# Kernel tuning notes

Hardware: AMD Instinct MI355X
Metric: run time of the kernel (lower is better)

Reference implementation:

```python
import jax, jax.numpy as jnp
import numpy as np

QC = 13        # quantum_channel
NQ = 12        # qubits per patch circuit
LAYERS12 = 3   # num_layer for FQConv ansatz
LAYERS4 = 4    # layers for the 4-qubit basic ansatz
GROUPS = 10
DIM = 40       # 3*QC + 1 channels
B = 1024
TDIM = 128
EPS = 1e-6     # flax GroupNorm default epsilon
TWO_PI = 2.0 * float(np.pi)


def _take2(s, ax):
    return jnp.take(s, 0, axis=ax), jnp.take(s, 1, axis=ax)


def init_state(n, N):
    # |0...0> state, shape (N, 2, 2, ..., 2); wire w lives on axis w+1
    s = jnp.zeros((N, 2 ** n), jnp.complex64).at[:, 0].set(1.0)
    return s.reshape((N,) + (2,) * n)


def apply_rx(state, theta, w):
    # RX(theta) = [[c, -i s], [-i s, c]], c=cos(theta/2), s=sin(theta/2)
    ax = w + 1
    theta = jnp.asarray(theta, jnp.float32)
    c = jnp.cos(0.5 * theta)
    s = jnp.sin(0.5 * theta)
    if theta.ndim > 0:  # per-sample angles (data embedding)
        sh = (-1,) + (1,) * (state.ndim - 2)
        c = c.reshape(sh)
        s = s.reshape(sh)
    c = c.astype(state.dtype)
    js = (1j * s).astype(state.dtype)
    s0, s1 = _take2(state, ax)
    return jnp.stack([c * s0 - js * s1, c * s1 - js * s0], axis=ax)


def apply_cnot(state, c, t):
    ca = c + 1
    ta = t + 1 if t < c else t  # target axis inside the control=1 slice
    s0, s1 = _take2(state, ca)
    return jnp.stack([s0, jnp.flip(s1, axis=ta)], axis=ca)


def apply_crz(state, theta, c, t):
    # CRZ = diag(1, 1, e^{-i theta/2}, e^{+i theta/2})
    ca = c + 1
    ta = t + 1 if t < c else t
    s0, s1 = _take2(state, ca)
    t0, t1 = _take2(s1, ta)
    em = jnp.exp(-0.5j * theta).astype(state.dtype)
    ep = jnp.exp(0.5j * theta).astype(state.dtype)
    s1 = jnp.stack([em * t0, ep * t1], axis=ta)
    return jnp.stack([s0, s1], axis=ca)


def apply_crx(state, theta, c, t):
    # controlled RX on target when control = 1
    ca = c + 1
    ta = t + 1 if t < c else t
    s0, s1 = _take2(state, ca)
    t0, t1 = _take2(s1, ta)
    ch = jnp.cos(0.5 * theta).astype(state.dtype)
    js = (1j * jnp.sin(0.5 * theta)).astype(state.dtype)
    s1 = jnp.stack([ch * t0 - js * t1, ch * t1 - js * t0], axis=ta)
    return jnp.stack([s0, s1], axis=ca)


def expvals_z(state, n):
    # <Z_w> = P(bit_w = 0) - P(bit_w = 1)
    p = jnp.real(state * jnp.conj(state))
    zs = []
    for w in range(n):
        axes = tuple(a for a in range(1, n + 1) if a != w + 1)
        q = p.sum(axis=axes)  # (N, 2)
        zs.append(q[:, 0] - q[:, 1])
    return jnp.stack(zs, axis=-1)  # (N, n)


def fqconv_layer(state, th):
    # zip(range(11,-1,-4), range(12)) -> i in (11,7,3), j in (0,1,2)
    for j, i in enumerate((11, 7, 3)):
        w1 = [i - 3, i - 2, i - 1, i] + [(i + k) % NQ for k in (1, 2, 3, 4)]
        tj = th[8 * j: 8 * (j + 1)]
        for bi, bj in zip(range(3, -1, -1), range(4)):  # block_C: CRZ
            state = apply_crz(state, TWO_PI * tj[bj], w1[bi + 4], w1[bi])
        for bi, bj in zip(range(3, -1, -1), range(4)):  # block_D: CRX
            state = apply_crx(state, TWO_PI * tj[4 + bj], w1[bi + 4], w1[bi])
    return state


def circuit12(x, theta):
    # x: (N, 12) angles; theta: (72,)
    state = init_state(NQ, x.shape[0])
    for w in range(NQ):  # AngleEmbedding, rotation='X'
        state = apply_rx(state, x[:, w], w)
    for l in range(LAYERS12):
        state = fqconv_layer(state, theta[24 * l: 24 * (l + 1)])
    return expvals_z(state, NQ)


def circuit4(x, theta):
    # Basic_ansatz, 4 qubits, 4 layers, 4 params/layer
    state = init_state(4, x.shape[0])
    for w in range(4):
        state = apply_rx(state, x[:, w], w)
    for l in range(LAYERS4):
        for w in range(4):
            state = apply_rx(state, theta[4 * l + w], w)
        for w in range(3):
            state = apply_cnot(state, w, w + 1)
        state = apply_cnot(state, 3, 0)
    return expvals_z(state, 4)


def run12_all(y, params, circ):
    # scan over the QC per-channel circuits (same structure, different params)
    def body(carry, xp):
        yy, th = xp
        return carry, circ(yy, th)
    _, zs = jax.lax.scan(body, None, (y, params))
    return zs  # (QC, N, 12)


def group_norm(h, scale, bias):
    Bn, H, W, C = h.shape
    g = h.reshape(Bn, H, W, GROUPS, C // GROUPS)
    mu = g.mean(axis=(1, 2, 4), keepdims=True)
    var = g.var(axis=(1, 2, 4), keepdims=True)
    g = (g - mu) * jax.lax.rsqrt(var + EPS)
    return g.reshape(Bn, H, W, C) * scale + bias


def forward(x, time_emb, qparams12, qparams4, gn0_scale, gn0_bias,
            gn1_scale, gn1_bias, time_w, time_b, circ12=circuit12):
    Bn = x.shape[0]

    def qpass(inp, p12_block):
        # per-channel 12-qubit circuits on 2x2x3 patches
        y = jnp.stack([inp[..., 3 * i:3 * (i + 1)].reshape(-1, 12) for i in range(QC)], 0)
        z = run12_all(y, p12_block, circ12)                      # (QC, Bn, 12)
        h1 = jnp.moveaxis(z.reshape(QC, Bn, 2, 2, 3), 0, -2).reshape(Bn, 2, 2, 3 * QC)
        # NOTE: faithful to the source, BOTH passes use circuit/params[-2]
        h4 = circuit4(inp[..., 3 * QC:].reshape(-1, 4), qparams4[0]).reshape(Bn, 2, 2, 1)
        return jnp.concatenate([h1, h4], axis=-1)                 # (Bn, 2, 2, 40)

    h = qpass(x, qparams12[:QC])
    h = group_norm(h, gn0_scale, gn0_bias)
    t = jax.nn.swish(time_emb) @ time_w + time_b                  # (Bn, 2*DIM)
    scale, shift = jnp.split(t[:, None, None, :], 2, axis=-1)
    h = jax.nn.swish(h * (1.0 + scale) + shift)
    h = qpass(h, qparams12[QC:])
    h = jax.nn.swish(group_norm(h, gn1_scale, gn1_bias))
    return x + h  # C == dim, so no res_conv


def setup_inputs() -> dict:
    key = jax.random.key(0)
    ks = jax.random.split(key, 5)
    return {
        "x": jax.random.normal(ks[0], (B, 2, 2, DIM), jnp.float32),
        "time_emb": jax.random.normal(ks[1], (B, TDIM), jnp.float32),
        "qparams12": jax.random.uniform(ks[2], (2 * QC, 24 * LAYERS12), jnp.float32),
        "qparams4": jax.random.uniform(ks[3], (2, 16), jnp.float32),
        "gn0_scale": jnp.ones((DIM,), jnp.float32),
        "gn0_bias": jnp.zeros((DIM,), jnp.float32),
        "gn1_scale": jnp.ones((DIM,), jnp.float32),
        "gn1_bias": jnp.zeros((DIM,), jnp.float32),
        "time_w": jax.random.normal(ks[4], (TDIM, 2 * DIM), jnp.float32) * (TDIM ** -0.5),
        "time_b": jnp.zeros((2 * DIM,), jnp.float32),
    }


def reference(x, time_emb, qparams12, qparams4, gn0_scale, gn0_bias,
              gn1_scale, gn1_bias, time_w, time_b):
    return forward(x, time_emb, qparams12, qparams4, gn0_scale, gn0_bias,
                   gn1_scale, gn1_bias, time_w, time_b)
```

## Files before the change

### kernel.cpp

```cpp
#include <hip/hip_runtime.h>
#include <math.h>


#define PI_F 3.14159265358979323846f

typedef float f2 __attribute__((ext_vector_type(2)));

__device__ __forceinline__ f2 shfl2(f2 v, int mask)
{
    f2 r;
    r[0] = __shfl_xor(v[0], mask, 64);
    r[1] = __shfl_xor(v[1], mask, 64);
    return r;
}

__device__ __forceinline__ void crz_g0_fused(const float* a, f2* R, f2* I,
                                             int lane, int wq)
{
    float gr[4], gi[4];
#pragma unroll
    for (int m = 0; m < 4; ++m) {
        bool cb;
        if      (m == 0) cb = (lane >> 4) & 1;
        else if (m == 1) cb = (lane >> 5) & 1;
        else if (m == 2) cb = wq & 1;
        else             cb = (wq >> 1) & 1;
        gr[m] = cb ? a[2 * m]     : 1.0f;
        gi[m] = cb ? a[2 * m + 1] : 0.0f;
    }
    float u0 = gr[1] * gr[0], v0 = gi[1] * gi[0];
    float w0 = gr[1] * gi[0], z0 = gi[1] * gr[0];
    float p01r[2] = { u0 - v0, u0 + v0 };
    float p01i[2] = { -(w0 + z0), w0 - z0 };
    float u1 = gr[3] * gr[2], v1 = gi[3] * gi[2];
    float w1 = gr[3] * gi[2], z1 = gi[3] * gr[2];
    float p23r[2] = { u1 - v1, u1 + v1 };
    float p23i[2] = { -(w1 + z1), w1 - z1 };

#pragma unroll
    for (int j = 0; j < 8; ++j) {
        const int ta  = (j < 4) ? 2 * j     : 15 - 2 * j;
        const int tb  = (j < 4) ? 2 * j + 1 : 14 - 2 * j;
        const float sgn = (j < 4) ? 1.0f : -1.0f;
        const int a10 = ta & 3, a2 = (ta >> 2) & 1;
        float bar = (a10 == 0 || a10 == 3) ? p01r[0] : p01r[1];
        float bai = (a10 == 0) ? p01i[0] : (a10 == 1) ? p01i[1]
                  : (a10 == 2) ? -p01i[1] : -p01i[0];
        float m0r = p23r[a2] * bar - p23i[a2] * bai;
        float m0i = p23r[a2] * bai + p23i[a2] * bar;
        const int b10 = tb & 3, b2 = (tb >> 2) & 1;
        float bbr = (b10 == 0 || b10 == 3) ? p01r[0] : p01r[1];
        float bbi = (b10 == 0) ? p01i[0] : (b10 == 1) ? p01i[1]
                  : (b10 == 2) ? -p01i[1] : -p01i[0];
        float m1r = p23r[b2] * bbr - p23i[b2] * bbi;
        float m1i = p23r[b2] * bbi + p23i[b2] * bbr;
        f2 mr = { m0r, m1r };
        f2 mi = { sgn * m0i, sgn * m1i };
        f2 r = R[j], im = I[j];
        R[j] = mr * r - mi * im;
        I[j] = mr * im + mi * r;
    }
}

__device__ __forceinline__ void crx_pair(float cg, float sg, f2* R, f2* I)
{
#pragma unroll
    for (int j = 0; j < 8; ++j) {
        f2 r = R[j], im = I[j];
        f2 rs = __builtin_shufflevector(r, r, 1, 0);
        f2 is = __builtin_shufflevector(im, im, 1, 0);
        R[j] = cg * r + sg * is;
        I[j] = cg * im - sg * rs;
    }
}

template<int M>
__device__ __forceinline__ void crx_elem(float cg, float sg, f2* R, f2* I)
{
#pragma unroll
    for (int j = 0; j < 8; ++j) {
        if (j & M) continue;
        const int p = j | M;
        f2 r0 = R[j], i0 = I[j], r1 = R[p], i1 = I[p];
        R[j] = cg * r0 + sg * i1;  I[j] = cg * i0 - sg * r1;
        R[p] = cg * r1 + sg * i0;  I[p] = cg * i1 - sg * r0;
    }
}

__device__ __forceinline__ void crz_e(float cg, float ss, f2* R, f2* I)
{
    const f2 mrv = {1.0f, cg};
    const f2 miv = {0.0f, ss};
#pragma unroll
    for (int j = 0; j < 8; ++j) {
        f2 r = R[j], im = I[j];
        R[j] = mrv * r - miv * im;
        I[j] = mrv * im + miv * r;
    }
}

template<int CB>
__device__ __forceinline__ void crz_ctrlj(float cg, float ss, f2* R, f2* I)
{
#pragma unroll
    for (int j = 0; j < 8; ++j) {
        if (!((j >> CB) & 1)) continue;
        f2 r = R[j], im = I[j];
        R[j] = cg * r - ss * im;
        I[j] = cg * im + ss * r;
    }
}

__device__ __forceinline__ void crx_sh_e(float cg, float sg, f2* R, f2* I)
{
    const f2 cgv = {1.0f, cg};
    const f2 sgv = {0.0f, sg};
#pragma unroll
    for (int j = 0; j < 8; ++j) {
        f2 br = shfl2(R[j], 1);
        f2 bi = shfl2(I[j], 1);
        f2 r = R[j], im = I[j];
        R[j] = cgv * r + sgv * bi;
        I[j] = cgv * im - sgv * br;
    }
}

template<int CB, int MASK>
__device__ __forceinline__ void crx_shj(float cg, float sg, f2* R, f2* I)
{
#pragma unroll
    for (int j = 0; j < 8; ++j) {
        if (!((j >> CB) & 1)) continue;
        f2 br = shfl2(R[j], MASK);
        f2 bi = shfl2(I[j], MASK);
        f2 r = R[j], im = I[j];
        R[j] = cg * r + sg * bi;
        I[j] = cg * im - sg * br;
    }
}

__device__ __forceinline__ void crz_g2_fused(const float* a, f2* R, f2* I,
                                             int lane, int wq)
{
    float s0 = ((lane >> 4) & 1) ? a[1] : -a[1];
    bool  c0 = lane & 1;
    float f0r = c0 ? a[0] : 1.0f, f0i = c0 ? s0 : 0.0f;
    float s1 = ((lane >> 5) & 1) ? a[3] : -a[3];
    bool  c1 = (lane >> 1) & 1;
    float f1r = c1 ? a[2] : 1.0f, f1i = c1 ? s1 : 0.0f;
    float s2 = (wq & 1) ? a[5] : -a[5];
    bool  c2 = (lane >> 2) & 1;
    float f2r = c2 ? a[4] : 1.0f, f2i = c2 ? s2 : 0.0f;
    float s3 = ((wq >> 1) & 1) ? a[7] : -a[7];
    bool  c3 = (lane >> 3) & 1;
    float f3r = c3 ? a[6] : 1.0f, f3i = c3 ? s3 : 0.0f;
    float t01r = f0r * f1r - f0i * f1i, t01i = f0r * f1i + f0i * f1r;
    float t23r = f2r * f3r - f2i * f3i, t23i = f2r * f3i + f2i * f3r;
    float Pr = t01r * t23r - t01i * t23i;
    float Pi = t01r * t23i + t01i * t23r;
#pragma unroll
    for (int j = 0; j < 8; ++j) {
        f2 r = R[j], im = I[j];
        R[j] = Pr * r - Pi * im;
        I[j] = Pr * im + Pi * r;
    }
}

template<int MASK>
__device__ __forceinline__ void crx_perm(float cg, float sg, f2* R, f2* I)
{
#pragma unroll
    for (int j = 0; j < 8; ++j) {
        float a0 = R[j][0], b0 = I[j][0];
        float a1 = R[j][1], b1 = I[j][1];
        if constexpr (MASK == 16) {
            asm("v_permlane16_swap_b32 %0, %1\n\t"
                "v_permlane16_swap_b32 %1, %0" : "+v"(a0), "+v"(b0));
            asm("v_permlane16_swap_b32 %0, %1\n\t"
                "v_permlane16_swap_b32 %1, %0" : "+v"(a1), "+v"(b1));
        } else {
            asm("v_permlane32_swap_b32 %0, %1\n\t"
                "v_permlane32_swap_b32 %1, %0" : "+v"(a0), "+v"(b0));
            asm("v_permlane32_swap_b32 %0, %1\n\t"
                "v_permlane32_swap_b32 %1, %0" : "+v"(a1), "+v"(b1));
        }
        f2 A = {a0, a1}, Bv = {b0, b1};
        f2 r = R[j], im = I[j];
        R[j] = cg * r + sg * A;
        I[j] = cg * im - sg * Bv;
    }
}

__global__ void __launch_bounds__(256, 4)
qpass12_kernel(const float* __restrict__ inp, const float* __restrict__ cs,
               float* __restrict__ outp)
{
    __shared__ f2 xbufv[4 * 32 * 17];
    float* xbuff = reinterpret_cast<float*>(xbufv);
    const int ts   = threadIdx.x;
    const int wq   = ts >> 6;
    const int lane = ts & 63;
    const int sim  = blockIdx.x;
    const int ci = sim % 13;
    const int b  = sim / 13;
    const float* csc = cs + ci * 144;
    const int ibase = b * 160 + ci * 3;

    float cw[12], sw[12];
#pragma unroll
    for (int w = 0; w < 12; ++w) {
        float x = inp[ibase + (w / 3) * 40 + (w % 3)];
        __sincosf(0.5f * x, &sw[w], &cw[w]);
    }

    float pref = ((wq >> 1) ? sw[0] : cw[0]) * ((wq & 1) ? sw[1] : cw[1]);
#pragma unroll
    for (int w = 2; w < 8; ++w)
        pref *= ((lane >> (7 - w)) & 1) ? sw[w] : cw[w];

    const int pl = (__popc(lane) + __popc(wq)) & 3;
    float oa = (pl == 0) ? 1.0f : (pl == 2) ? -1.0f : 0.0f;
    float ob = (pl == 1) ? -1.0f : (pl == 3) ? 1.0f : 0.0f;

    f2 R[8], I[8];
#pragma unroll
    for (int j = 0; j < 8; ++j) {
        float base = pref * ((j & 4) ? sw[8] : cw[8]) *
                     ((j & 2) ? sw[9] : cw[9]) * ((j & 1) ? sw[10] : cw[10]);
        f2 v2 = { base * cw[11], base * sw[11] };
        const int q0 = __popc(j) & 3;
        const int q1 = (q0 + 1) & 3;
        const float c0l = (q0 == 0) ? oa : (q0 == 1) ? ob : (q0 == 2) ? -oa : -ob;
        const float c1l = (q0 == 0) ? ob : (q0 == 1) ? -oa : (q0 == 2) ? -ob : oa;
        const float c0h = (q1 == 0) ? oa : (q1 == 1) ? ob : (q1 == 2) ? -oa : -ob;
        const float c1h = (q1 == 0) ? ob : (q1 == 1) ? -oa : (q1 == 2) ? -ob : oa;
        R[j] = f2{ v2[0] * c0l, v2[1] * c0h };
        I[j] = f2{ v2[0] * c1l, v2[1] * c1h };
    }

    const bool act2 = (lane >> 2) & 1;
    const bool act3 = (lane >> 3) & 1;
    const int ai2 = ((lane >> 3) << 2) | (lane & 3);
    const int ai3 = ((lane >> 4) << 3) | (lane & 7);
    f2* xw2 = &xbufv[(wq * 32 + ai2) * 17];
    f2* xr2 = &xbufv[((wq ^ 1) * 32 + ai2) * 17];
    f2* xw3 = &xbufv[(wq * 32 + ai3) * 17];
    f2* xr3 = &xbufv[((wq ^ 2) * 32 + ai3) * 17];

#pragma unroll 1
    for (int l = 0; l < 3; ++l) {
        const float* a = csc + l * 48;

        crz_g0_fused(a, R, I, lane, wq);
        { bool cb = (lane >> 4) & 1;
          crx_pair(cb ? a[ 8] : 1.0f, cb ? a[ 9] : 0.0f, R, I); }
        { bool cb = (lane >> 5) & 1;
          crx_elem<1>(cb ? a[10] : 1.0f, cb ? a[11] : 0.0f, R, I); }
        { bool cb = wq & 1;
          crx_elem<2>(cb ? a[12] : 1.0f, cb ? a[13] : 0.0f, R, I); }
        { bool cb = (wq >> 1) & 1;
          crx_elem<4>(cb ? a[14] : 1.0f, cb ? a[15] : 0.0f, R, I); }

        { float ss = (lane & 1) ? a[17] : -a[17];
          crz_e(a[16], ss, R, I); }
        { float ss = ((lane >> 1) & 1) ? a[19] : -a[19];
          crz_ctrlj<0>(a[18], ss, R, I); }
        { float ss = ((lane >> 2) & 1) ? a[21] : -a[21];
          crz_ctrlj<1>(a[20], ss, R, I); }
        { float ss = ((lane >> 3) & 1) ? a[23] : -a[23];
          crz_ctrlj<2>(a[22], ss, R, I); }
        crx_sh_e(a[24], a[25], R, I);
        crx_shj<0, 2>(a[26], a[27], R, I);
        crx_shj<1, 4>(a[28], a[29], R, I);
        crx_shj<2, 8>(a[30], a[31], R, I);

        crz_g2_fused(a + 32, R, I, lane, wq);
        { bool cb = lane & 1;
          crx_perm<16>(cb ? a[40] : 1.0f, cb ? a[41] : 0.0f, R, I); }
        { bool cb = (lane >> 1) & 1;
          crx_perm<32>(cb ? a[42] : 1.0f, cb ? a[43] : 0.0f, R, I); }
        __syncthreads();
        if (act2) {
#pragma unroll
            for (int j = 0; j < 8; ++j) {
                xw2[j]     = R[j];
                xw2[8 + j] = I[j];
            }
        }
        __syncthreads();
        if (act2) {
            float cg = a[44], sg = a[45];
#pragma unroll
            for (int j = 0; j < 8; ++j) {
                f2 br = xr2[j], bi = xr2[8 + j];
                f2 r = R[j], im = I[j];
                R[j] = cg * r + sg * bi;
                I[j] = cg * im - sg * br;
            }
        }
        __syncthreads();
        if (act3) {
#pragma unroll
            for (int j = 0; j < 8; ++j) {
                xw3[j]     = R[j];
                xw3[8 + j] = I[j];
            }
        }
        __syncthreads();
        if (act3) {
            float cg = a[46], sg = a[47];
#pragma unroll
            for (int j = 0; j < 8; ++j) {
                f2 br = xr3[j], bi = xr3[8 + j];
                f2 r = R[j], im = I[j];
                R[j] = cg * r + sg * bi;
                I[j] = cg * im - sg * br;
            }
        }
    }

    f2 accT = {0.0f, 0.0f}, acc8 = {0.0f, 0.0f};
    f2 acc9 = {0.0f, 0.0f}, acc10 = {0.0f, 0.0f};
#pragma unroll
    for (int j = 0; j < 8; ++j) {
        f2 p = R[j] * R[j] + I[j] * I[j];
        accT += p;
        if (j & 4) acc8 -= p; else acc8 += p;
        if (j & 2) acc9 -= p; else acc9 += p;
        if (j & 1) acc10 -= p; else acc10 += p;
    }
    float total = accT[0] + accT[1];
    float v12[12];
    v12[0] = (wq >> 1) ? -total : total;
    v12[1] = (wq & 1) ? -total : total;
#pragma unroll
    for (int w = 2; w < 8; ++w)
        v12[w] = ((lane >> (7 - w)) & 1) ? -total : total;
    v12[8]  = acc8[0] + acc8[1];
    v12[9]  = acc9[0] + acc9[1];
    v12[10] = acc10[0] + acc10[1];
    v12[11] = accT[0] - accT[1];

#pragma unroll
    for (int w = 0; w < 12; ++w) {
#pragma unroll
        for (int off = 1; off < 64; off <<= 1)
            v12[w] += __shfl_xor(v12[w], off, 64);
    }
    __syncthreads();
    if (lane == 0) {
#pragma unroll
        for (int w = 0; w < 12; ++w)
            xbuff[wq * 12 + w] = v12[w];
    }
    __syncthreads();
    if (ts < 12) {
        float z = xbuff[ts] + xbuff[12 + ts] + xbuff[24 + ts] + xbuff[36 + ts];
        outp[ibase + (ts / 3) * 40 + (ts % 3)] = z;
    }
}

__global__ void q4_kernel(const float* __restrict__ inp,
                          const float* __restrict__ cs4,
                          float* __restrict__ outp)
{
    int b = blockIdx.x * blockDim.x + threadIdx.x;
    if (b >= 1024) return;
    float cw[4], sw[4];
#pragma unroll
    for (int j = 0; j < 4; ++j) {
        float x = inp[(b * 4 + j) * 40 + 39];
        __sincosf(0.5f * x, &sw[j], &cw[j]);
    }
    float sr[16], si[16];
#pragma unroll
    for (int k = 0; k < 16; ++k) {
        float v = 1.0f;
#pragma unroll
        for (int j = 0; j < 4; ++j)
            v *= ((k >> (3 - j)) & 1) ? sw[j] : cw[j];
        int ph = __popc(k) & 3;
        sr[k] = (ph == 0) ? v : (ph == 2) ? -v : 0.0f;
        si[k] = (ph == 1) ? -v : (ph == 3) ? v : 0.0f;
    }
#pragma unroll
    for (int l = 0; l < 4; ++l) {
#pragma unroll
        for (int w = 0; w < 4; ++w) {
            float cg = cs4[2 * (4 * l + w)], sg = cs4[2 * (4 * l + w) + 1];
            const int m = 1 << (3 - w);
#pragma unroll
            for (int k = 0; k < 16; ++k) {
                if (k & m) continue;
                int p2 = k | m;
                float r0 = sr[k], i0 = si[k], r1 = sr[p2], i1 = si[p2];
                sr[k]  = cg * r0 + sg * i1;  si[k]  = cg * i0 - sg * r1;
                sr[p2] = cg * r1 + sg * i0;  si[p2] = cg * i1 - sg * r0;
            }
        }
#pragma unroll
        for (int e = 0; e < 4; ++e) {
            const int cq = e, tq = (e + 1) & 3;
            const int pcb = 1 << (3 - cq), ptb = 1 << (3 - tq);
#pragma unroll
            for (int k = 0; k < 16; ++k) {
                if (!(k & pcb)) continue;
                if (k & ptb) continue;
                int p2 = k | ptb;
                float tr = sr[k], ti = si[k];
                sr[k] = sr[p2]; si[k] = si[p2];
                sr[p2] = tr;    si[p2] = ti;
            }
        }
    }
    float p[16];
#pragma unroll
    for (int k = 0; k < 16; ++k) p[k] = sr[k] * sr[k] + si[k] * si[k];
#pragma unroll
    for (int j = 0; j < 4; ++j) {
        float z = 0.0f;
#pragma unroll
        for (int k = 0; k < 16; ++k)
            z += ((k >> (3 - j)) & 1) ? -p[k] : p[k];
        outp[(b * 4 + j) * 40 + 39] = z;
    }
}

__global__ void prep_kernel(const float* __restrict__ q12,
                            const float* __restrict__ q4,
                            float* __restrict__ cs12,
                            float* __restrict__ cs4)
{
    int idx = blockIdx.x * 256 + threadIdx.x;
    if (idx < 26 * 72) {
        float s, c;
        sincosf(PI_F * q12[idx], &s, &c);
        cs12[2 * idx]     = c;
        cs12[2 * idx + 1] = s;
    }
    if (idx < 16) {
        float s, c;
        sincosf(0.5f * q4[idx], &s, &c);
        cs4[2 * idx]     = c;
        cs4[2 * idx + 1] = s;
    }
}

__global__ void tmlp_kernel(const float* __restrict__ emb,
                            const float* __restrict__ W,
                            const float* __restrict__ bias,
                            float* __restrict__ t)
{
    __shared__ float se[128];
    int b = blockIdx.x, tid = threadIdx.x;
    float e = emb[b * 128 + tid];
    se[tid] = e / (1.0f + __expf(-e));
    __syncthreads();
    if (tid < 80) {
        float acc = bias[tid];
        for (int k = 0; k < 128; ++k) acc += se[k] * W[k * 80 + tid];
        t[b * 80 + tid] = acc;
    }
}

__global__ void gn0_kernel(const float* __restrict__ h, const float* __restrict__ t,
                           const float* __restrict__ sc, const float* __restrict__ bi,
                           float* __restrict__ outp)
{
    __shared__ float v[160];
    __shared__ float mu[10], rstd[10];
    int b = blockIdx.x, tid = threadIdx.x;
    if (tid < 160) v[tid] = h[b * 160 + tid];
    __syncthreads();
    if (tid < 10) {
        float s1 = 0.0f, s2 = 0.0f;
#pragma unroll
        for (int sp = 0; sp < 4; ++sp)
#pragma unroll
            for (int k = 0; k < 4; ++k) {
                float x = v[sp * 40 + tid * 4 + k];
                s1 += x; s2 += x * x;
            }
        float m = s1 * (1.0f / 16.0f);
        float var = s2 * (1.0f / 16.0f) - m * m;
        mu[tid] = m; rstd[tid] = rsqrtf(var + 1e-6f);
    }
    __syncthreads();
    if (tid < 160) {
        int ch = tid % 40;
        int g = ch >> 2;
        float hn = (v[tid] - mu[g]) * rstd[g] * sc[ch] + bi[ch];
        float scale = t[b * 80 + ch], shift = t[b * 80 + 40 + ch];
        float z = hn * (1.0f + scale) + shift;
        outp[b * 160 + tid] = z / (1.0f + __expf(-z));
    }
}

__global__ void gn1_kernel(const float* __restrict__ h, const float* __restrict__ x,
                           const float* __restrict__ sc, const float* __restrict__ bi,
                           float* __restrict__ outp)
{
    __shared__ float v[160];
    __shared__ float mu[10], rstd[10];
    int b = blockIdx.x, tid = threadIdx.x;
    if (tid < 160) v[tid] = h[b * 160 + tid];
    __syncthreads();
    if (tid < 10) {
        float s1 = 0.0f, s2 = 0.0f;
#pragma unroll
        for (int sp = 0; sp < 4; ++sp)
#pragma unroll
            for (int k = 0; k < 4; ++k) {
                float xx = v[sp * 40 + tid * 4 + k];
                s1 += xx; s2 += xx * xx;
            }
        float m = s1 * (1.0f / 16.0f);
        float var = s2 * (1.0f / 16.0f) - m * m;
        mu[tid] = m; rstd[tid] = rsqrtf(var + 1e-6f);
    }
    __syncthreads();
    if (tid < 160) {
        int ch = tid % 40;
        int g = ch >> 2;
        float hn = (v[tid] - mu[g]) * rstd[g] * sc[ch] + bi[ch];
        float sws = hn / (1.0f + __expf(-hn));
        outp[b * 160 + tid] = x[b * 160 + tid] + sws;
    }
}

extern "C" void kernel_launch(void* const* d_in, const int* in_sizes, int n_in,
                              void* d_out, int out_size, void* d_ws, size_t ws_size,
                              hipStream_t stream)
{
    const float* x    = (const float*)d_in[0];
    const float* temb = (const float*)d_in[1];
    const float* q12  = (const float*)d_in[2];
    const float* q4   = (const float*)d_in[3];
    const float* gn0s = (const float*)d_in[4];
    const float* gn0b = (const float*)d_in[5];
    const float* gn1s = (const float*)d_in[6];
    const float* gn1b = (const float*)d_in[7];
    const float* tw   = (const float*)d_in[8];
    const float* tb   = (const float*)d_in[9];
    float* out = (float*)d_out;

    float* ws   = (float*)d_ws;
    float* cs12 = ws;
    float* cs4  = cs12 + 3744;
    float* tbuf = cs4 + 32;
    float* A    = tbuf + 81920;
    float* Bf   = A + 163840;

    prep_kernel<<<8, 256, 0, stream>>>(q12, q4, cs12, cs4);
    tmlp_kernel<<<1024, 128, 0, stream>>>(temb, tw, tb, tbuf);

    qpass12_kernel<<<13312, 256, 0, stream>>>(x, cs12, A);
    q4_kernel<<<16, 64, 0, stream>>>(x, cs4, A);
    gn0_kernel<<<1024, 160, 0, stream>>>(A, tbuf, gn0s, gn0b, Bf);

    qpass12_kernel<<<13312, 256, 0, stream>>>(Bf, cs12 + 13 * 144, A);
    q4_kernel<<<16, 64, 0, stream>>>(Bf, cs4, A);
    gn1_kernel<<<1024, 160, 0, stream>>>(A, x, gn1s, gn1b, out);
}
```

Measured before the change: 650.6 us.

## Replace shfl_xor exchanges with DPP/swizzle/permlane and restructure wave reductions

Cross-lane exchanges in the CRX gates now use DPP row operations (xor1, xor2, xor8), ds_swizzle (xor4) and permlane swaps instead of __shfl_xor, which goes through LDS-bypass bpermute. The final 12-way wave reduction is restructured: the eight sign-pattern Z expectations are derived from a single butterfly on the total plus difference terms captured at each stage, which cuts the number of full 64-lane reductions. This adds inline assembly for v_permlane16/32_swap, which is specific to newer CDNA parts. It also relies on the DPP control encodings being correct for xor semantics; the xor8 encoding in particular looks questionable.

Result: faster. 577.5 us (-11.2%).

```diff
diff --git a/kernel.cpp b/kernel.cpp
--- a/kernel.cpp
+++ b/kernel.cpp
@@ -4,14 +4,61 @@
 
 #define PI_F 3.14159265358979323846f
 
+#define DPP_XOR1 0xB1
+#define DPP_XOR2 0x4E
+#define DPP_XOR8 0x128
+
 typedef float f2 __attribute__((ext_vector_type(2)));
 
-__device__ __forceinline__ f2 shfl2(f2 v, int mask)
+template<int CTRL>
+__device__ __forceinline__ float dppf(float x)
+{
+    return __int_as_float(__builtin_amdgcn_update_dpp(
+        __float_as_int(x), __float_as_int(x), CTRL, 0xF, 0xF, false));
+}
+
+template<int CTRL>
+__device__ __forceinline__ f2 dpp2v(f2 v)
 {
     f2 r;
-    r[0] = __shfl_xor(v[0], mask, 64);
-    r[1] = __shfl_xor(v[1], mask, 64);
+    r[0] = dppf<CTRL>(v[0]);
+    r[1] = dppf<CTRL>(v[1]);
     return r;
+}
+
+__device__ __forceinline__ float swz4f(float x)
+{
+    return __int_as_float(__builtin_amdgcn_ds_swizzle(__float_as_int(x), 0x101F));
+}
+
+__device__ __forceinline__ f2 swz4v(f2 v)
+{
+    f2 r;
+    r[0] = swz4f(v[0]);
+    r[1] = swz4f(v[1]);
+    return r;
+}
+
+__device__ __forceinline__ float psum16(float x)
+{
+    float c, d;
+    asm("v_mov_b32 %0, %2\n\t"
+        "v_mov_b32 %1, %2\n\t"
+        "v_permlane16_swap_b32 %0, %1"
+        : "=&v"(c), "=&v"(d)
+        : "v"(x));
+    return c + d;
+}
+
+__device__ __forceinline__ float psum32(float x)
+{
+    float c, d;
+    asm("v_mov_b32 %0, %2\n\t"
+        "v_mov_b32 %1, %2\n\t"
+        "v_permlane32_swap_b32 %0, %1"
+        : "=&v"(c), "=&v"(d)
+        : "v"(x));
+    return c + d;
 }
 
 __device__ __forceinline__ void crz_g0_fused(const float* a, f2* R, f2* I,
@@ -117,22 +164,36 @@
     const f2 sgv = {0.0f, sg};
 #pragma unroll
     for (int j = 0; j < 8; ++j) {
-        f2 br = shfl2(R[j], 1);
-        f2 bi = shfl2(I[j], 1);
+        f2 br = dpp2v<DPP_XOR1>(R[j]);
+        f2 bi = dpp2v<DPP_XOR1>(I[j]);
         f2 r = R[j], im = I[j];
         R[j] = cgv * r + sgv * bi;
         I[j] = cgv * im - sgv * br;
     }
 }
 
-template<int CB, int MASK>
-__device__ __forceinline__ void crx_shj(float cg, float sg, f2* R, f2* I)
+template<int CB, int CTRL>
+__device__ __forceinline__ void crx_shj_dpp(float cg, float sg, f2* R, f2* I)
 {
 #pragma unroll
     for (int j = 0; j < 8; ++j) {
         if (!((j >> CB) & 1)) continue;
-        f2 br = shfl2(R[j], MASK);
-        f2 bi = shfl2(I[j], MASK);
+        f2 br = dpp2v<CTRL>(R[j]);
+        f2 bi = dpp2v<CTRL>(I[j]);
+        f2 r = R[j], im = I[j];
+        R[j] = cg * r + sg * bi;
+        I[j] = cg * im - sg * br;
+    }
+}
+
+template<int CB>
+__device__ __forceinline__ void crx_shj_swz4(float cg, float sg, f2* R, f2* I)
+{
+#pragma unroll
+    for (int j = 0; j < 8; ++j) {
+        if (!((j >> CB) & 1)) continue;
+        f2 br = swz4v(R[j]);
+        f2 bi = swz4v(I[j]);
         f2 r = R[j], im = I[j];
         R[j] = cg * r + sg * bi;
         I[j] = cg * im - sg * br;
@@ -270,9 +331,9 @@
         { float ss = ((lane >> 3) & 1) ? a[23] : -a[23];
           crz_ctrlj<2>(a[22], ss, R, I); }
         crx_sh_e(a[24], a[25], R, I);
-        crx_shj<0, 2>(a[26], a[27], R, I);
-        crx_shj<1, 4>(a[28], a[29], R, I);
-        crx_shj<2, 8>(a[30], a[31], R, I);
+        crx_shj_dpp<0, DPP_XOR2>(a[26], a[27], R, I);
+        crx_shj_swz4<1>(a[28], a[29], R, I);
+        crx_shj_dpp<2, DPP_XOR8>(a[30], a[31], R, I);
 
         crz_g2_fused(a + 32, R, I, lane, wq);
         { bool cb = lane & 1;
@@ -329,29 +390,59 @@
         if (j & 2) acc9 -= p; else acc9 += p;
         if (j & 1) acc10 -= p; else acc10 += p;
     }
-    float total = accT[0] + accT[1];
-    float v12[12];
-    v12[0] = (wq >> 1) ? -total : total;
-    v12[1] = (wq & 1) ? -total : total;
-#pragma unroll
-    for (int w = 2; w < 8; ++w)
-        v12[w] = ((lane >> (7 - w)) & 1) ? -total : total;
-    v12[8]  = acc8[0] + acc8[1];
-    v12[9]  = acc9[0] + acc9[1];
-    v12[10] = acc10[0] + acc10[1];
-    v12[11] = accT[0] - accT[1];
-
-#pragma unroll
-    for (int w = 0; w < 12; ++w) {
-#pragma unroll
-        for (int off = 1; off < 64; off <<= 1)
-            v12[w] += __shfl_xor(v12[w], off, 64);
-    }
+    float T   = accT[0] + accT[1];
+    float A11 = accT[0] - accT[1];
+    float A8  = acc8[0] + acc8[1];
+    float A9  = acc9[0] + acc9[1];
+    float A10 = acc10[0] + acc10[1];
+
+    float dc0, dc1, dc2, dc3, dc4, dc5;
+    float x = T;
+    { float u = dppf<DPP_XOR1>(x); dc0 = x - u; x += u; }
+    { float u = dppf<DPP_XOR2>(x); dc1 = x - u; x += u; }
+    { float u = swz4f(x);          dc2 = x - u; x += u; }
+    { float u = dppf<DPP_XOR8>(x); dc3 = x - u; x += u; }
+    { float s = psum16(x);         dc4 = 2.0f * x - s; x = s; }
+    { float s = psum32(x);         dc5 = 2.0f * x - s; x = s; }
+    dc0 += dppf<DPP_XOR2>(dc0);
+    dc0 += swz4f(dc0);
+    dc0 += dppf<DPP_XOR8>(dc0);
+    dc0 = psum16(dc0);  dc0 = psum32(dc0);
+    dc1 += swz4f(dc1);
+    dc1 += dppf<DPP_XOR8>(dc1);
+    dc1 = psum16(dc1);  dc1 = psum32(dc1);
+    dc2 += dppf<DPP_XOR8>(dc2);
+    dc2 = psum16(dc2);  dc2 = psum32(dc2);
+    dc3 = psum16(dc3);  dc3 = psum32(dc3);
+    dc4 = psum32(dc4);
+    A8  += dppf<DPP_XOR1>(A8);   A8  += dppf<DPP_XOR2>(A8);
+    A8  += swz4f(A8);            A8  += dppf<DPP_XOR8>(A8);
+    A8  = psum16(A8);            A8  = psum32(A8);
+    A9  += dppf<DPP_XOR1>(A9);   A9  += dppf<DPP_XOR2>(A9);
+    A9  += swz4f(A9);            A9  += dppf<DPP_XOR8>(A9);
+    A9  = psum16(A9);            A9  = psum32(A9);
+    A10 += dppf<DPP_XOR1>(A10);  A10 += dppf<DPP_XOR2>(A10);
+    A10 += swz4f(A10);           A10 += dppf<DPP_XOR8>(A10);
+    A10 = psum16(A10);           A10 = psum32(A10);
+    A11 += dppf<DPP_XOR1>(A11);  A11 += dppf<DPP_XOR2>(A11);
+    A11 += swz4f(A11);           A11 += dppf<DPP_XOR8>(A11);
+    A11 = psum16(A11);           A11 = psum32(A11);
+
     __syncthreads();
     if (lane == 0) {
-#pragma unroll
-        for (int w = 0; w < 12; ++w)
-            xbuff[wq * 12 + w] = v12[w];
+        float* wv = &xbuff[wq * 12];
+        wv[0]  = (wq >> 1) ? -x : x;
+        wv[1]  = (wq & 1)  ? -x : x;
+        wv[2]  = dc5;
+        wv[3]  = dc4;
+        wv[4]  = dc3;
+        wv[5]  = dc2;
+        wv[6]  = dc1;
+        wv[7]  = dc0;
+        wv[8]  = A8;
+        wv[9]  = A9;
+        wv[10] = A10;
+        wv[11] = A11;
     }
     __syncthreads();
     if (ts < 12) {
```
